# Kernel optimization log

Measured on AMD Instinct MI355X. Metric: run time of the kernel, lower is better.

Reference implementation:

```python
import jax, jax.numpy as jnp
import numpy as np
import math

B, T, D = 2, 2048, 2048
H, DH = 16, 128
DKV, DQ, DR = 512, 1024, 64
ROPE_BASE = 500000.0
EPS = 1e-6
SCALE = 1.0 / math.sqrt(DH + DR)


def setup_inputs() -> dict:
    key = jax.random.key(0)
    ks = jax.random.split(key, 12)
    s = 0.02
    return {
        'x': jax.random.normal(ks[0], (B, T, D), jnp.float32),
        'W_DQ': jax.random.normal(ks[1], (D, DQ), jnp.float32) * s,
        'W_UQ': jax.random.normal(ks[2], (DQ, H * DH), jnp.float32) * s,
        'W_QR': jax.random.normal(ks[3], (DQ, H * DR), jnp.float32) * s,
        'W_DKV': jax.random.normal(ks[4], (D, DKV), jnp.float32) * s,
        'W_UK': jax.random.normal(ks[5], (DKV, H * DH), jnp.float32) * s,
        'W_UV': jax.random.normal(ks[6], (DKV, H * DH), jnp.float32) * s,
        'W_KR': jax.random.normal(ks[7], (D, DR), jnp.float32) * s,
        'W_O': jax.random.normal(ks[8], (H * DH, D), jnp.float32) * s,
        'q_norm_w': jnp.ones((DQ,), jnp.float32),
        'kv_norm_w': jnp.ones((DKV,), jnp.float32),
    }


def _rmsnorm(v, w):
    n = jax.lax.rsqrt(jnp.mean(v * v, axis=-1, keepdims=True) + EPS)
    return v * n * w


def _rotate_half(v):
    v1, v2 = jnp.split(v, 2, axis=-1)
    return jnp.concatenate([-v2, v1], axis=-1)


def _rope_tables(seq_len):
    inv_freq = 1.0 / (ROPE_BASE ** (jnp.arange(0, DR, 2, dtype=jnp.float32) / DR))
    t = jnp.arange(seq_len, dtype=jnp.float32)
    freqs = jnp.outer(t, inv_freq)              # (S, DR/2)
    emb = jnp.concatenate([freqs, freqs], -1)   # (S, DR)
    return jnp.cos(emb), jnp.sin(emb)


def reference(x, W_DQ, W_UQ, W_QR, W_DKV, W_UK, W_UV, W_KR, W_O, q_norm_w, kv_norm_w):
    # Query path: low-rank compress -> RMSNorm -> up-project (content + rope parts)
    c_Q = _rmsnorm(x @ W_DQ, q_norm_w)                               # (B,T,DQ)
    q_C = (c_Q @ W_UQ).reshape(B, T, H, DH).transpose(0, 2, 1, 3)    # (B,H,T,DH)
    q_R = (c_Q @ W_QR).reshape(B, T, H, DR).transpose(0, 2, 1, 3)    # (B,H,T,DR)
    # KV path: joint low-rank latent + decoupled rope key
    c_KV = _rmsnorm(x @ W_DKV, kv_norm_w)                            # (B,T,DKV)
    k_C = (c_KV @ W_UK).reshape(B, T, H, DH).transpose(0, 2, 1, 3)   # (B,H,T,DH)
    v_C = (c_KV @ W_UV).reshape(B, T, H, DH).transpose(0, 2, 1, 3)   # (B,H,T,DH)
    k_R = (x @ W_KR)[:, None, :, :]                                  # (B,1,T,DR) shared across heads
    # Decoupled RoPE
    cos, sin = _rope_tables(T)
    cos = cos[None, None]; sin = sin[None, None]                     # (1,1,T,DR)
    q_R = q_R * cos + _rotate_half(q_R) * sin
    k_R = k_R * cos + _rotate_half(k_R) * sin
    k_R = jnp.broadcast_to(k_R, (B, H, T, DR))
    q = jnp.concatenate([q_C, q_R], axis=-1)                         # (B,H,T,DH+DR)
    k = jnp.concatenate([k_C, k_R], axis=-1)
    # Causal attention with MLA scale 1/sqrt(d_head + d_rope)
    scores = jnp.einsum('bhqd,bhkd->bhqk', q, k) * SCALE
    causal = jnp.tril(jnp.ones((T, T), bool))
    scores = jnp.where(causal, scores, jnp.finfo(scores.dtype).min)
    attn = jax.nn.softmax(scores, axis=-1)
    out = jnp.einsum('bhqk,bhkd->bhqd', attn, v_C)                   # (B,H,T,DH)
    out = out.transpose(0, 2, 1, 3).reshape(B, T, H * DH)
    return out @ W_O                                                 # (B,T,D)
```

## Files before the change

### kernel.cpp

```cpp
#include <hip/hip_runtime.h>
#include <cstdint>
#include <cstddef>

#define B_   2
#define T_   2048
#define D_   2048
#define H_   16
#define DH_  128
#define DQ_  1024
#define DKV_ 512
#define DR_  64
#define M_   4096
#define SCALE_ 0.07216878364870323f
#define SC2_   0.10412808709930322f
#define LN_BASE_ 13.122363377404328f

typedef unsigned short u16;
typedef __attribute__((ext_vector_type(8))) short short8;
typedef __attribute__((ext_vector_type(4))) float f32x4;

__device__ __forceinline__ float b2f(u16 u) { return __uint_as_float(((uint32_t)u) << 16); }
__device__ __forceinline__ u16 f2b(float f) {
    uint32_t x = __float_as_uint(f);
    return (u16)((x + 0x7fffu + ((x >> 16) & 1u)) >> 16);
}
__device__ __forceinline__ u16 f2b_fast(float f) {
    return (u16)((__float_as_uint(f) + 0x8000u) >> 16);
}

__device__ __forceinline__ void gload_lds16(const u16* src, u16* dst) {
    __builtin_amdgcn_global_load_lds(
        (const __attribute__((address_space(1))) uint32_t*)(uintptr_t)src,
        (__attribute__((address_space(3))) uint32_t*)(uintptr_t)dst, 16, 0, 0);
}

struct TPack {
    const float* src[8];
    u16*         dst[8];
    int K[8];
    int N[8];
    int ntx[8];
    int start[9];
};

__global__ __launch_bounds__(256) void prep_k(TPack p, const float* __restrict__ x,
                                              u16* __restrict__ xb, int ntr) {
    const int bid = blockIdx.x;
    if (bid < ntr) {
        __shared__ float tile[32][33];
        int w = 0;
#pragma unroll
        for (int i = 1; i < 8; ++i) if (bid >= p.start[i]) w = i;
        const int lt = bid - p.start[w];
        const int bx = lt % p.ntx[w], by = lt / p.ntx[w];
        const float* in = p.src[w];
        u16* out = p.dst[w];
        const int K = p.K[w], N = p.N[w];
        const int k0 = by * 32, n0 = bx * 32;
        const int tx = threadIdx.x & 31, ty = threadIdx.x >> 5;
#pragma unroll
        for (int i = 0; i < 4; ++i) {
            int k = k0 + ty + i * 8;
            int n = n0 + tx;
            tile[ty + i * 8][tx] = (n < N) ? in[(size_t)k * N + n] : 0.f;
        }
        __syncthreads();
#pragma unroll
        for (int i = 0; i < 4; ++i) {
            int n = n0 + ty + i * 8;
            out[(size_t)n * K + k0 + tx] = f2b(tile[tx][ty + i * 8]);
        }
    } else {
        const int i = ((bid - ntr) * 256 + threadIdx.x) * 4;
        const float4 v = *(const float4*)(x + i);
        ushort4 o;
        o.x = f2b(v.x); o.y = f2b(v.y); o.z = f2b(v.z); o.w = f2b(v.w);
        *(ushort4*)(xb + i) = o;
    }
}

template <int OUT_BF16>
__global__ __launch_bounds__(256) void gemm_tn(const u16* __restrict__ A,
                                               const u16* __restrict__ Bt,
                                               void* __restrict__ Cv,
                                               int N, int K) {
    __shared__ __attribute__((aligned(16))) u16 lA[128 * 32];
    __shared__ __attribute__((aligned(16))) u16 lB[128 * 32];
    const int m0 = blockIdx.y * 128, n0 = blockIdx.x * 128;
    const int tid = threadIdx.x, wave = tid >> 6, lane = tid & 63;
    const int wm = (wave >> 1) * 64, wn = (wave & 1) * 64;
    const int r = lane & 15, kq = lane >> 4;

    f32x4 acc[4][4];
#pragma unroll
    for (int i = 0; i < 4; ++i)
#pragma unroll
        for (int j = 0; j < 4; ++j) acc[i][j] = (f32x4){0.f, 0.f, 0.f, 0.f};

    for (int kk = 0; kk < K; kk += 32) {
#pragma unroll
        for (int p = 0; p < 2; ++p) {
            const int c = p * 256 + wave * 64 + lane;
            const u16* ga = A  + (size_t)(m0 + (c >> 2)) * K + kk + (c & 3) * 8;
            const u16* gb = Bt + (size_t)(n0 + (c >> 2)) * K + kk + (c & 3) * 8;
            u16* la = lA + (size_t)(p * 256 + wave * 64) * 8;
            u16* lb = lB + (size_t)(p * 256 + wave * 64) * 8;
            gload_lds16(ga, la);
            gload_lds16(gb, lb);
        }
        __syncthreads();
        short8 av[4], bv[4];
#pragma unroll
        for (int mi = 0; mi < 4; ++mi)
            av[mi] = *(const short8*)&lA[(wm + mi * 16 + r) * 32 + kq * 8];
#pragma unroll
        for (int ni = 0; ni < 4; ++ni)
            bv[ni] = *(const short8*)&lB[(wn + ni * 16 + r) * 32 + kq * 8];
#pragma unroll
        for (int mi = 0; mi < 4; ++mi)
#pragma unroll
            for (int ni = 0; ni < 4; ++ni)
                acc[mi][ni] = __builtin_amdgcn_mfma_f32_16x16x32_bf16(
                    av[mi], bv[ni], acc[mi][ni], 0, 0, 0);
        __syncthreads();
    }
    const int r4 = (lane >> 4) * 4, cc = lane & 15;
#pragma unroll
    for (int mi = 0; mi < 4; ++mi)
#pragma unroll
        for (int ni = 0; ni < 4; ++ni)
#pragma unroll
            for (int i = 0; i < 4; ++i) {
                const int row = m0 + wm + mi * 16 + r4 + i;
                const int col = n0 + wn + ni * 16 + cc;
                const float v = acc[mi][ni][i];
                if (OUT_BF16) ((u16*)Cv)[(size_t)row * N + col] = f2b(v);
                else          ((float*)Cv)[(size_t)row * N + col] = v;
            }
}

#define S_BM 256
#define S_BN 256
#define S_BK 64

__device__ __forceinline__ void gemm256_core(
    const u16* __restrict__ A, const u16* __restrict__ Bt, int K,
    int m0, int n0, int tid, f32x4 (&acc)[8][4],
    u16 (*sA)[S_BM * S_BK], u16 (*sB)[S_BN * S_BK]) {
    const int lane = tid & 63;
    const int wave = tid >> 6;
    const int wm = wave >> 2;
    const int r = lane & 15, kq = lane >> 4;
    const int wn = wave & 3;

    const u16* gA[4]; const u16* gB[4]; int dOf[4];
#pragma unroll
    for (int is = 0; is < 4; ++is) {
        const int c = is * 512 + tid;
        const int row = c >> 3, c16 = c & 7;
        gA[is] = A  + (size_t)(m0 + row) * K + ((c16 ^ (row & 7)) * 8);
        gB[is] = Bt + (size_t)(n0 + row) * K + ((c16 ^ (row & 7)) * 8);
        dOf[is] = c * 8;
    }

    const int NKT = K >> 6;

    auto STG = [&](int arr, int half, int bs, int kk) {
        u16* dst = arr ? (u16*)sB[bs] : (u16*)sA[bs];
        const u16** g = arr ? gB : gA;
#pragma unroll
        for (int is = half * 2; is < half * 2 + 2; ++is)
            gload_lds16(g[is] + kk, dst + dOf[is]);
    };

    STG(0, 0, 0, 0); STG(0, 1, 0, 0); STG(1, 0, 0, 0); STG(1, 1, 0, 0);

    short8 af[4][2], bf[2][2];
    for (int kt = 0; kt < NKT; ++kt) {
        const int cur = kt & 1;
        const int kk = (kt + 1) * 64;
        const int pf = (kt + 1 < NKT);
        const u16* cA = sA[cur];
        const u16* cB = sB[cur];

        auto lda = [&](int row, int g) -> short8 {
            return *(const short8*)&cA[row * 64 + ((g ^ (row & 7)) * 8)];
        };
        auto ldb = [&](int row, int g) -> short8 {
            return *(const short8*)&cB[row * 64 + ((g ^ (row & 7)) * 8)];
        };

#pragma unroll
        for (int ph = 0; ph < 4; ++ph) {
            const int mh = ph >> 1;
            const int nh = (ph == 1 || ph == 2) ? 1 : 0;
            if (pf) STG(ph >> 1, ph & 1, cur ^ 1, kk);
            if (ph == 0) {
                if (pf) asm volatile("s_waitcnt vmcnt(2)" ::: "memory");
                else    asm volatile("s_waitcnt vmcnt(0)" ::: "memory");
            }
            __builtin_amdgcn_s_barrier();
            asm volatile("" ::: "memory");
            if (!(ph & 1)) {
#pragma unroll
                for (int mi = 0; mi < 4; ++mi)
#pragma unroll
                    for (int ks = 0; ks < 2; ++ks)
                        af[mi][ks] = lda(wm * 128 + mh * 64 + mi * 16 + r, ks * 4 + kq);
            }
#pragma unroll
            for (int ni = 0; ni < 2; ++ni)
#pragma unroll
                for (int ks = 0; ks < 2; ++ks)
                    bf[ni][ks] = ldb(wn * 64 + nh * 32 + ni * 16 + r, ks * 4 + kq);
#pragma unroll
            for (int ks = 0; ks < 2; ++ks)
#pragma unroll
                for (int mi = 0; mi < 4; ++mi)
#pragma unroll
                    for (int ni = 0; ni < 2; ++ni)
                        acc[mh * 4 + mi][nh * 2 + ni] =
                            __builtin_amdgcn_mfma_f32_16x16x32_bf16(
                                af[mi][ks], bf[ni][ks],
                                acc[mh * 4 + mi][nh * 2 + ni], 0, 0, 0);
            asm volatile("" ::: "memory");
            __builtin_amdgcn_s_barrier();
            asm volatile("" ::: "memory");
        }
    }
}

__global__ __launch_bounds__(512, 1) void gemm256p_k(
    const u16* __restrict__ A0, const u16* __restrict__ B0,
    u16* __restrict__ C0, int N0c, int K0,
    const u16* __restrict__ A1, const u16* __restrict__ B1,
    u16* __restrict__ C1, int N1c, int K1,
    u16* __restrict__ Vt, int vcol0, int nx0)
{
    __shared__ __attribute__((aligned(16))) u16 sA[2][S_BM * S_BK];
    __shared__ __attribute__((aligned(16))) u16 sB[2][S_BN * S_BK];
    const int sel = (int)blockIdx.x >= nx0;
    const u16* A  = sel ? A1 : A0;
    const u16* Bt = sel ? B1 : B0;
    const int  K  = sel ? K1 : K0;
    const int lbx = sel ? (blockIdx.x - nx0) : blockIdx.x;
    const int m0 = blockIdx.y * S_BM, n0 = lbx * S_BN;
    const int tid = threadIdx.x, lane = tid & 63;
    const int wave = tid >> 6, wm = wave >> 2, wn = wave & 3;
    const int kq = lane >> 4;

    f32x4 acc[8][4];
#pragma unroll
    for (int i = 0; i < 8; ++i)
#pragma unroll
        for (int j = 0; j < 4; ++j) acc[i][j] = (f32x4){0.f, 0.f, 0.f, 0.f};

    gemm256_core(A, Bt, K, m0, n0, tid, acc, sA, sB);

    const int r4c = kq * 4, cc = lane & 15;
    if (!sel) {
#pragma unroll
        for (int mf = 0; mf < 8; ++mf)
#pragma unroll
            for (int nf = 0; nf < 4; ++nf)
#pragma unroll
                for (int i = 0; i < 4; ++i) {
                    const int row = m0 + wm * 128 + mf * 16 + r4c + i;
                    const int col = n0 + wn * 64 + nf * 16 + cc;
                    C0[(size_t)row * N0c + col] = f2b(acc[mf][nf][i]);
                }
    } else if (n0 < vcol0) {
#pragma unroll
        for (int mf = 0; mf < 8; ++mf)
#pragma unroll
            for (int nf = 0; nf < 4; ++nf)
#pragma unroll
                for (int i = 0; i < 4; ++i) {
                    const int row = m0 + wm * 128 + mf * 16 + r4c + i;
                    const int col = n0 + wn * 64 + nf * 16 + cc;
                    C1[(size_t)row * N1c + col] = f2b(acc[mf][nf][i]);
                }
    } else {
#pragma unroll
        for (int mf = 0; mf < 8; ++mf)
#pragma unroll
            for (int nf = 0; nf < 4; ++nf) {
                const int tp = m0 + wm * 128 + mf * 16 + r4c;
                const int c  = n0 - vcol0 + wn * 64 + nf * 16 + cc;
                u16 tmp[4];
#pragma unroll
                for (int i = 0; i < 4; ++i) tmp[i] = f2b(acc[mf][nf][i]);
                *(ushort4*)&Vt[((size_t)((tp >> 11) * 2048 + c)) * 2048 + (tp & 2047)]
                    = *(ushort4*)tmp;
            }
    }
}

__global__ __launch_bounds__(256) void normrope_k(const u16* __restrict__ P1,
                                                  const float* __restrict__ qnw,
                                                  const float* __restrict__ kvnw,
                                                  u16* __restrict__ cQb,
                                                  u16* __restrict__ cKVb,
                                                  u16* __restrict__ kRb) {
    const int which = blockIdx.y;
    if (which < 2) {
        const int row = blockIdx.x;
        const int N = which ? 512 : 1024;
        const int off = which ? 1024 : 0;
        const float* w = which ? kvnw : qnw;
        u16* outp = which ? cKVb : cQb;
        const u16* src = P1 + (size_t)row * 1664 + off;
        const int j = threadIdx.x * 4;
        float v[4] = {0.f, 0.f, 0.f, 0.f};
        if (j < N) {
            ushort4 u = *(const ushort4*)(src + j);
            v[0] = b2f(u.x); v[1] = b2f(u.y); v[2] = b2f(u.z); v[3] = b2f(u.w);
        }
        float ss = v[0]*v[0] + v[1]*v[1] + v[2]*v[2] + v[3]*v[3];
#pragma unroll
        for (int offc = 32; offc; offc >>= 1) ss += __shfl_down(ss, offc);
        __shared__ float red[4];
        const int wave = threadIdx.x >> 6, lane = threadIdx.x & 63;
        if (lane == 0) red[wave] = ss;
        __syncthreads();
        const float tot = red[0] + red[1] + red[2] + red[3];
        const float sc = rsqrtf(tot / (float)N + 1e-6f);
        if (j < N) {
            ushort4 o;
            o.x = f2b(v[0] * sc * w[j]);
            o.y = f2b(v[1] * sc * w[j + 1]);
            o.z = f2b(v[2] * sc * w[j + 2]);
            o.w = f2b(v[3] * sc * w[j + 3]);
            *(ushort4*)(outp + (size_t)row * N + j) = o;
        }
    } else {
        if (blockIdx.x >= 1024) return;
        const int row = blockIdx.x * 4 + (threadIdx.x >> 6);
        const int j = threadIdx.x & 63;
        const int t = row & (T_ - 1);
        const int i = j & 31;
        const float invf = __expf(-LN_BASE_ * (float)(2 * i) * (1.0f / 64.0f));
        const float ang = (float)t * invf;
        const float c = cosf(ang), s = sinf(ang);
        const u16* src = P1 + (size_t)row * 1664 + 1536;
        const float v = b2f(src[j]);
        const float rot = (j < 32) ? -b2f(src[j + 32]) : b2f(src[j - 32]);
        kRb[(size_t)row * 64 + j] = f2b(v * c + rot * s);
    }
}

#define ABQ  128
#define ABK  64
#define NW   8
#define KSTR 192
#define VSTR 64
#define PSTR 64
#define VOFF 12288
#define KVSZ 20480
#define QSTRIDE 3072
#define KSTRIDE 4096

__global__ __launch_bounds__(512, 1) void attn_mfma_k(
    const u16* __restrict__ qC,
    const u16* __restrict__ kC, const u16* __restrict__ kR,
    const u16* __restrict__ Vt, u16* __restrict__ outp)
{
    __shared__ __attribute__((aligned(16))) u16 sKV[3][KVSZ];
    __shared__ __attribute__((aligned(16))) u16 sP[NW * 16 * PSTR];

    const int h = blockIdx.x, b = blockIdx.z;
    const int qb = b ? (15 - (int)blockIdx.y) : (int)blockIdx.y;
    const int q0 = qb * ABQ;
    const int tid = threadIdx.x, wave = tid >> 6, lane = tid & 63;
    const int r = lane & 15, kq = lane >> 4, r4 = kq * 4;
    const int wq = wave * 16;

    const u16* gsrc[5]; int gstep[5]; int doff[5];
#pragma unroll
    for (int j = 0; j < 5; ++j) {
        const int i = wave + NW * j;
        if (i < 24) {
            const int s = i * 64 + lane;
            const int rr2 = s / 24;
            const int cc = s - rr2 * 24;
            const int scc = cc ^ (rr2 & 7);
            if (scc < 16) {
                gsrc[j] = kC + (size_t)(b * T_ + rr2) * KSTRIDE + h * 128 + scc * 8;
                gstep[j] = ABK * KSTRIDE;
            } else {
                gsrc[j] = kR + (size_t)(b * T_ + rr2) * 64 + (scc - 16) * 8;
                gstep[j] = ABK * 64;
            }
            doff[j] = i * 512;
        } else {
            const int iv = i - 24;
            const int s = iv * 64 + lane;
            const int rr2 = s >> 3;
            const int cc = s & 7;
            const int scc = cc ^ (rr2 & 7);
            gsrc[j] = Vt + ((size_t)(b * H_ + h) * 128 + rr2) * T_ + scc * 8;
            gstep[j] = ABK;
            doff[j] = VOFF + iv * 512;
        }
    }

    short8 qf[6];
    {
        const int t = q0 + wq + r;
        const u16* qcrow = qC + (size_t)(b * T_ + t) * QSTRIDE + h * 128 + kq * 8;
#pragma unroll
        for (int kc = 0; kc < 4; ++kc) qf[kc] = *(const short8*)(qcrow + kc * 32);
        const u16* qrraw = qC + (size_t)(b * T_ + t) * QSTRIDE + 2048 + h * 64 + kq * 8;
        const short8 q0v = *(const short8*)(qrraw);
        const short8 q1v = *(const short8*)(qrraw + 32);
        short8 o0, o1;
#pragma unroll
        for (int j = 0; j < 8; ++j) {
            const int i = kq * 8 + j;
            const float invf = __expf(-LN_BASE_ * (float)(2 * i) * (1.0f / 64.0f));
            const float ang = (float)t * invf;
            const float cs = cosf(ang), sn = sinf(ang);
            const float a = b2f((u16)q0v[j]), bb = b2f((u16)q1v[j]);
            o0[j] = (short)f2b(a * cs - bb * sn);
            o1[j] = (short)f2b(bb * cs + a * sn);
        }
        qf[4] = o0; qf[5] = o1;
    }

    f32x4 Oa[8];
#pragma unroll
    for (int nt = 0; nt < 8; ++nt) Oa[nt] = (f32x4){0.f, 0.f, 0.f, 0.f};
    float Lrow[4] = {0.f, 0.f, 0.f, 0.f};

    u16* myP = sP + (size_t)wave * 16 * PSTR;
    const int re = r & 7;

    auto STAGE = [&](int kt2, int bs) {
        u16* dst = &sKV[bs][0];
#pragma unroll
        for (int j = 0; j < 5; ++j)
            gload_lds16(gsrc[j] + (size_t)kt2 * (size_t)gstep[j], dst + doff[j]);
    };

    const int nkt = 2 * qb + 2;
    STAGE(0, 0);
    STAGE(1, 1);
    for (int kt = 0; kt < nkt; ++kt) {
        const int cur = kt % 3;
        if (kt == 0 || kt >= nkt - 1) {
            asm volatile("s_waitcnt vmcnt(0)" ::: "memory");
        } else {
            asm volatile("s_waitcnt vmcnt(5)" ::: "memory");
        }
        __builtin_amdgcn_s_barrier();
        asm volatile("" ::: "memory");

        const u16* cK = &sKV[cur][0];
        const u16* cV = &sKV[cur][VOFF];
        const int k0 = kt * ABK;

        f32x4 Sa[4];
#pragma unroll
        for (int nt = 0; nt < 4; ++nt) Sa[nt] = (f32x4){0.f, 0.f, 0.f, 0.f};
#pragma unroll
        for (int kc = 0; kc < 6; ++kc) {
            short8 kf[4];
#pragma unroll
            for (int nt = 0; nt < 4; ++nt)
                kf[nt] = *(const short8*)&cK[(nt * 16 + r) * KSTR
                                            + (((kc * 4 + kq) ^ re) * 8)];
#pragma unroll
            for (int nt = 0; nt < 4; ++nt)
                Sa[nt] = __builtin_amdgcn_mfma_f32_16x16x32_bf16(
                    qf[kc], kf[nt], Sa[nt], 0, 0, 0);
        }

        if (kt < nkt - 2) {
#pragma unroll
            for (int i = 0; i < 4; ++i) {
                const int prow = r4 + i;
                const int pre = prow & 7;
                float sm = 0.f;
#pragma unroll
                for (int nt = 0; nt < 4; ++nt) {
                    const float p = exp2f(Sa[nt][i] * SC2_);
                    sm += p;
                    myP[prow * PSTR + (((nt * 2 + (r >> 3)) ^ pre) * 8) + re]
                        = f2b_fast(p);
                }
                Lrow[i] += sm;
            }
        } else {
#pragma unroll
            for (int i = 0; i < 4; ++i) {
                const int prow = r4 + i;
                const int pre = prow & 7;
                const int grow = q0 + wq + prow;
                float sm = 0.f;
#pragma unroll
                for (int nt = 0; nt < 4; ++nt) {
                    float p = exp2f(Sa[nt][i] * SC2_);
                    p = (k0 + nt * 16 + r > grow) ? 0.f : p;
                    sm += p;
                    myP[prow * PSTR + (((nt * 2 + (r >> 3)) ^ pre) * 8) + re]
                        = f2b_fast(p);
                }
                Lrow[i] += sm;
            }
        }

#pragma unroll
        for (int kc2 = 0; kc2 < 2; ++kc2) {
            const short8 pf = *(const short8*)&myP[r * PSTR
                                                  + (((kc2 * 4 + kq) ^ re) * 8)];
#pragma unroll
            for (int nt = 0; nt < 8; ++nt) {
                const short8 vf = *(const short8*)&cV[(nt * 16 + r) * VSTR
                                                     + (((kc2 * 4 + kq) ^ re) * 8)];
                Oa[nt] = __builtin_amdgcn_mfma_f32_16x16x32_bf16(
                    pf, vf, Oa[nt], 0, 0, 0);
            }
        }

        if (kt + 2 < nkt) STAGE(kt + 2, (kt + 2) % 3);
    }

#pragma unroll
    for (int i = 0; i < 4; ++i) {
        float L = Lrow[i];
        L += __shfl_xor(L, 1);
        L += __shfl_xor(L, 2);
        L += __shfl_xor(L, 4);
        L += __shfl_xor(L, 8);
        const float inv = 1.0f / L;
        const int t = q0 + wq + r4 + i;
        u16* orow = outp + (size_t)(b * T_ + t) * 2048 + h * 128;
#pragma unroll
        for (int nt = 0; nt < 8; ++nt)
            orow[nt * 16 + r] = f2b(Oa[nt][i] * inv);
    }
}

extern "C" void kernel_launch(void* const* d_in, const int* in_sizes, int n_in,
                              void* d_out, int out_size, void* d_ws, size_t ws_size,
                              hipStream_t stream) {
    (void)in_sizes; (void)n_in; (void)out_size; (void)ws_size;
    const float* x     = (const float*)d_in[0];
    const float* W_DQ  = (const float*)d_in[1];
    const float* W_UQ  = (const float*)d_in[2];
    const float* W_QR  = (const float*)d_in[3];
    const float* W_DKV = (const float*)d_in[4];
    const float* W_UK  = (const float*)d_in[5];
    const float* W_UV  = (const float*)d_in[6];
    const float* W_KR  = (const float*)d_in[7];
    const float* W_O   = (const float*)d_in[8];
    const float* qnw   = (const float*)d_in[9];
    const float* kvnw  = (const float*)d_in[10];
    float* out = (float*)d_out;

    char* base = (char*)d_ws;
    size_t o = 0;
    auto alloc = [&](size_t bytes) {
        char* r = base + o;
        o += (bytes + 255) & ~(size_t)255;
        return r;
    };
    u16* WT1  = (u16*)alloc((size_t)1664 * 2048 * 2);
    u16* WT2  = (u16*)alloc((size_t)3072 * 1024 * 2);
    u16* WT3  = (u16*)alloc((size_t)4096 * 512 * 2);
    u16* WT_O = (u16*)alloc((size_t)2048 * 2048 * 2);
    u16* xb   = (u16*)alloc((size_t)M_ * 2048 * 2);
    u16* U1   = (u16*)alloc((size_t)M_ * 2048 * 2);
    u16* P2   = (u16*)alloc((size_t)M_ * 3072 * 2);
    u16* P3   = (u16*)alloc((size_t)M_ * 4096 * 2);
    u16* cQb  = (u16*)alloc((size_t)M_ * 1024 * 2);
    u16* cKVb = (u16*)alloc((size_t)M_ * 512 * 2);
    u16* qRb  = (u16*)alloc((size_t)M_ * 1024 * 2);
    u16* kRb  = (u16*)alloc((size_t)M_ * 64 * 2);
    (void)qRb;
    u16* P1       = U1;
    u16* attn_out = U1;
    u16* Vt       = xb;

    TPack tp;
    const float* srcs[8] = {W_DQ, W_DKV, W_KR, W_UQ, W_QR, W_UK, W_UV, W_O};
    u16* dsts[8] = {WT1, WT1 + (size_t)1024*2048, WT1 + (size_t)1536*2048,
                    WT2, WT2 + (size_t)2048*1024,
                    WT3, WT3 + (size_t)2048*512, WT_O};
    const int Ks[8]   = {2048, 2048, 2048, 1024, 1024, 512, 512, 2048};
    const int Ns[8]   = {1024,  512,   64, 2048, 1024, 2048, 2048, 2048};
    const int ntxs[8] = {  32,   16,    4,   64,   32,   64,   64,   64};
    int cum = 0;
    for (int i = 0; i < 8; ++i) {
        tp.src[i] = srcs[i]; tp.dst[i] = dsts[i];
        tp.K[i] = Ks[i]; tp.N[i] = Ns[i]; tp.ntx[i] = ntxs[i];
        tp.start[i] = cum;
        cum += ntxs[i] * (Ks[i] / 32);
    }
    tp.start[8] = cum;
    const int ncast = (M_ * D_) / 1024;
    prep_k<<<cum + ncast, 256, 0, stream>>>(tp, x, xb, cum);

    gemm_tn<1><<<dim3(1664/128, M_/128), 256, 0, stream>>>(xb, WT1, (void*)P1, 1664, 2048);

    normrope_k<<<dim3(M_, 3), 256, 0, stream>>>(P1, qnw, kvnw, cQb, cKVb, kRb);

    gemm256p_k<<<dim3(3072/256 + 4096/256, M_/256), 512, 0, stream>>>(
        cQb,  WT2, P2, 3072, 1024,
        cKVb, WT3, P3, 4096, 512,
        Vt, 2048, 3072/256);

    attn_mfma_k<<<dim3(H_, T_/ABQ, B_), 512, 0, stream>>>(P2, P3, kRb, Vt, attn_out);

    gemm_tn<0><<<dim3(2048/128, M_/128), 256, 0, stream>>>(attn_out, WT_O, (void*)out, 2048, 2048);
}
```

Baseline: 388.6 us.

## Replace simple 128x128 GEMM with double-buffered 256x128 swizzled GEMM

Swaps the basic 128x128 single-buffered GEMM used for the down-projection and output projection for a new 512-thread 256x128 kernel. The new kernel double-buffers LDS with prefetch of the next K tile, uses an XOR-swizzled LDS layout to avoid bank conflicts, and uses BK=64. This aims to hide global load latency and raise MFMA utilisation. The trade-off is fewer blocks (e.g. 13x16=208 for the first GEMM), which may underfill the CUs.

Result: faster. 354.8 us (-8.7%).

```diff
diff --git a/kernel.cpp b/kernel.cpp
--- a/kernel.cpp
+++ b/kernel.cpp
@@ -79,66 +79,6 @@
     }
 }
 
-template <int OUT_BF16>
-__global__ __launch_bounds__(256) void gemm_tn(const u16* __restrict__ A,
-                                               const u16* __restrict__ Bt,
-                                               void* __restrict__ Cv,
-                                               int N, int K) {
-    __shared__ __attribute__((aligned(16))) u16 lA[128 * 32];
-    __shared__ __attribute__((aligned(16))) u16 lB[128 * 32];
-    const int m0 = blockIdx.y * 128, n0 = blockIdx.x * 128;
-    const int tid = threadIdx.x, wave = tid >> 6, lane = tid & 63;
-    const int wm = (wave >> 1) * 64, wn = (wave & 1) * 64;
-    const int r = lane & 15, kq = lane >> 4;
-
-    f32x4 acc[4][4];
-#pragma unroll
-    for (int i = 0; i < 4; ++i)
-#pragma unroll
-        for (int j = 0; j < 4; ++j) acc[i][j] = (f32x4){0.f, 0.f, 0.f, 0.f};
-
-    for (int kk = 0; kk < K; kk += 32) {
-#pragma unroll
-        for (int p = 0; p < 2; ++p) {
-            const int c = p * 256 + wave * 64 + lane;
-            const u16* ga = A  + (size_t)(m0 + (c >> 2)) * K + kk + (c & 3) * 8;
-            const u16* gb = Bt + (size_t)(n0 + (c >> 2)) * K + kk + (c & 3) * 8;
-            u16* la = lA + (size_t)(p * 256 + wave * 64) * 8;
-            u16* lb = lB + (size_t)(p * 256 + wave * 64) * 8;
-            gload_lds16(ga, la);
-            gload_lds16(gb, lb);
-        }
-        __syncthreads();
-        short8 av[4], bv[4];
-#pragma unroll
-        for (int mi = 0; mi < 4; ++mi)
-            av[mi] = *(const short8*)&lA[(wm + mi * 16 + r) * 32 + kq * 8];
-#pragma unroll
-        for (int ni = 0; ni < 4; ++ni)
-            bv[ni] = *(const short8*)&lB[(wn + ni * 16 + r) * 32 + kq * 8];
-#pragma unroll
-        for (int mi = 0; mi < 4; ++mi)
-#pragma unroll
-            for (int ni = 0; ni < 4; ++ni)
-                acc[mi][ni] = __builtin_amdgcn_mfma_f32_16x16x32_bf16(
-                    av[mi], bv[ni], acc[mi][ni], 0, 0, 0);
-        __syncthreads();
-    }
-    const int r4 = (lane >> 4) * 4, cc = lane & 15;
-#pragma unroll
-    for (int mi = 0; mi < 4; ++mi)
-#pragma unroll
-        for (int ni = 0; ni < 4; ++ni)
-#pragma unroll
-            for (int i = 0; i < 4; ++i) {
-                const int row = m0 + wm + mi * 16 + r4 + i;
-                const int col = n0 + wn + ni * 16 + cc;
-                const float v = acc[mi][ni][i];
-                if (OUT_BF16) ((u16*)Cv)[(size_t)row * N + col] = f2b(v);
-                else          ((float*)Cv)[(size_t)row * N + col] = v;
-            }
-}
-
 #define S_BM 256
 #define S_BN 256
 #define S_BK 64
@@ -228,6 +168,128 @@
             asm volatile("" ::: "memory");
         }
     }
+}
+
+#define N_BM 256
+#define N_BN 128
+#define N_BK 64
+
+template <int OUT_BF16>
+__global__ __launch_bounds__(512, 1) void gemm256n_k(const u16* __restrict__ A,
+                                                     const u16* __restrict__ Bt,
+                                                     void* __restrict__ Cv,
+                                                     int N, int K) {
+    __shared__ __attribute__((aligned(16))) u16 sA[2][N_BM * N_BK];
+    __shared__ __attribute__((aligned(16))) u16 sB[2][N_BN * N_BK];
+    const int m0 = blockIdx.y * N_BM, n0 = blockIdx.x * N_BN;
+    const int tid = threadIdx.x, lane = tid & 63, wave = tid >> 6;
+    const int wm = wave >> 2, wn = wave & 3;
+    const int r = lane & 15, kq = lane >> 4;
+
+    const u16* gA[4]; int dOfA[4];
+    const u16* gB[2]; int dOfB[2];
+#pragma unroll
+    for (int is = 0; is < 4; ++is) {
+        const int c = is * 512 + tid;
+        const int row = c >> 3, c16 = c & 7;
+        gA[is] = A + (size_t)(m0 + row) * K + ((c16 ^ (row & 7)) * 8);
+        dOfA[is] = c * 8;
+    }
+#pragma unroll
+    for (int is = 0; is < 2; ++is) {
+        const int c = is * 512 + tid;
+        const int row = c >> 3, c16 = c & 7;
+        gB[is] = Bt + (size_t)(n0 + row) * K + ((c16 ^ (row & 7)) * 8);
+        dOfB[is] = c * 8;
+    }
+
+    f32x4 acc[8][2];
+#pragma unroll
+    for (int i = 0; i < 8; ++i)
+#pragma unroll
+        for (int j = 0; j < 2; ++j) acc[i][j] = (f32x4){0.f, 0.f, 0.f, 0.f};
+
+    const int NKT = K >> 6;
+
+    auto STGA = [&](int half, int bs, int kk) {
+#pragma unroll
+        for (int is = half * 2; is < half * 2 + 2; ++is)
+            gload_lds16(gA[is] + kk, (u16*)sA[bs] + dOfA[is]);
+    };
+    auto STGB = [&](int bs, int kk) {
+#pragma unroll
+        for (int is = 0; is < 2; ++is)
+            gload_lds16(gB[is] + kk, (u16*)sB[bs] + dOfB[is]);
+    };
+
+    STGA(0, 0, 0); STGA(1, 0, 0); STGB(0, 0);
+
+    short8 af[4][2], bf[2];
+    for (int kt = 0; kt < NKT; ++kt) {
+        const int cur = kt & 1;
+        const int kk = (kt + 1) * 64;
+        const int pf = (kt + 1 < NKT);
+        const u16* cA = sA[cur];
+        const u16* cB = sB[cur];
+
+        auto lda = [&](int row, int g) -> short8 {
+            return *(const short8*)&cA[row * 64 + ((g ^ (row & 7)) * 8)];
+        };
+        auto ldb = [&](int row, int g) -> short8 {
+            return *(const short8*)&cB[row * 64 + ((g ^ (row & 7)) * 8)];
+        };
+
+#pragma unroll
+        for (int ph = 0; ph < 4; ++ph) {
+            const int mh = ph >> 1;
+            const int nh = (ph == 1 || ph == 2) ? 1 : 0;
+            if (pf) {
+                if (ph == 0)      STGA(0, cur ^ 1, kk);
+                else if (ph == 1) STGA(1, cur ^ 1, kk);
+                else if (ph == 2) STGB(cur ^ 1, kk);
+            }
+            if (ph == 0) {
+                if (pf) asm volatile("s_waitcnt vmcnt(2)" ::: "memory");
+                else    asm volatile("s_waitcnt vmcnt(0)" ::: "memory");
+            }
+            __builtin_amdgcn_s_barrier();
+            asm volatile("" ::: "memory");
+            if (!(ph & 1)) {
+#pragma unroll
+                for (int mi = 0; mi < 4; ++mi)
+#pragma unroll
+                    for (int ks = 0; ks < 2; ++ks)
+                        af[mi][ks] = lda(wm * 128 + mh * 64 + mi * 16 + r, ks * 4 + kq);
+            }
+#pragma unroll
+            for (int ks = 0; ks < 2; ++ks)
+                bf[ks] = ldb(wn * 32 + nh * 16 + r, ks * 4 + kq);
+#pragma unroll
+            for (int ks = 0; ks < 2; ++ks)
+#pragma unroll
+                for (int mi = 0; mi < 4; ++mi)
+                    acc[mh * 4 + mi][nh] =
+                        __builtin_amdgcn_mfma_f32_16x16x32_bf16(
+                            af[mi][ks], bf[ks], acc[mh * 4 + mi][nh], 0, 0, 0);
+            asm volatile("" ::: "memory");
+            __builtin_amdgcn_s_barrier();
+            asm volatile("" ::: "memory");
+        }
+    }
+
+    const int r4c = kq * 4, cc = lane & 15;
+#pragma unroll
+    for (int mf = 0; mf < 8; ++mf)
+#pragma unroll
+        for (int nf = 0; nf < 2; ++nf)
+#pragma unroll
+            for (int i = 0; i < 4; ++i) {
+                const int row = m0 + wm * 128 + mf * 16 + r4c + i;
+                const int col = n0 + wn * 32 + nf * 16 + cc;
+                const float v = acc[mf][nf][i];
+                if (OUT_BF16) ((u16*)Cv)[(size_t)row * N + col] = f2b(v);
+                else          ((float*)Cv)[(size_t)row * N + col] = v;
+            }
 }
 
 __global__ __launch_bounds__(512, 1) void gemm256p_k(
@@ -601,7 +663,8 @@
     const int ncast = (M_ * D_) / 1024;
     prep_k<<<cum + ncast, 256, 0, stream>>>(tp, x, xb, cum);
 
-    gemm_tn<1><<<dim3(1664/128, M_/128), 256, 0, stream>>>(xb, WT1, (void*)P1, 1664, 2048);
+    gemm256n_k<1><<<dim3(1664/128, M_/256), 512, 0, stream>>>(
+        xb, WT1, (void*)P1, 1664, 2048);
 
     normrope_k<<<dim3(M_, 3), 256, 0, stream>>>(P1, qnw, kvnw, cQb, cKVb, kRb);
 
@@ -612,5 +675,6 @@
 
     attn_mfma_k<<<dim3(H_, T_/ABQ, B_), 512, 0, stream>>>(P2, P3, kRb, Vt, attn_out);
 
-    gemm_tn<0><<<dim3(2048/128, M_/128), 256, 0, stream>>>(attn_out, WT_O, (void*)out, 2048, 2048);
-}
+    gemm256n_k<0><<<dim3(2048/128, M_/256), 512, 0, stream>>>(
+        attn_out, WT_O, (void*)out, 2048, 2048);
+}
```
